# Optimization experiments

Hardware: AMD Instinct MI355X
Metric: run time of the kernel (lower is better)

Reference implementation:

```python
import jax, jax.numpy as jnp
import numpy as np

N = 100000   # nodes
E = 2500000  # edges (before self-loops)
G = 64       # graphs in the batch


def _glorot(key, fi, fo):
    return jax.random.normal(key, (fi, fo), jnp.float32) * jnp.sqrt(2.0 / (fi + fo))


def setup_inputs() -> dict:
    key = jax.random.key(0)
    ks = jax.random.split(key, 8)
    x = jax.random.normal(ks[0], (N, 3), jnp.float32)
    edge_index = jax.random.randint(ks[1], (2, E), 0, N)
    batch = jnp.sort(jax.random.randint(ks[2], (N,), 0, G))
    return dict(
        x=x, edge_index=edge_index, batch=batch,
        W1=_glorot(ks[3], 3, 16),  b1=jnp.zeros((16,), jnp.float32),
        W2=_glorot(ks[4], 16, 32), b2=jnp.zeros((32,), jnp.float32),
        W3=_glorot(ks[5], 32, 16), b3=jnp.zeros((16,), jnp.float32),
        W4=_glorot(ks[6], 16, 2),  b4=jnp.zeros((2,), jnp.float32),
    )


def reference(x, edge_index, batch, W1, b1, W2, b2, W3, b3, W4, b4):
    # PyG GCNConv: add self-loops, sym-normalize by deg^{-1/2}, gather->scatter-add.
    loops = jnp.arange(N)
    src = jnp.concatenate([edge_index[0], loops])  # [E+N]
    dst = jnp.concatenate([edge_index[1], loops])
    deg = jax.ops.segment_sum(jnp.ones_like(dst, jnp.float32), dst, num_segments=N)
    dinv = jax.lax.rsqrt(jnp.maximum(deg, 1.0))  # deg >= 1 due to self-loops
    norm = (dinv[src] * dinv[dst])[:, None]      # [E+N, 1]

    def gcn_conv(h, W, b):
        h = h @ W                                  # [N, out]
        msg = h[src] * norm                        # gather + edge scaling
        agg = jax.ops.segment_sum(msg, dst, num_segments=N)  # scatter-add
        return agg + b

    h = jax.nn.relu(gcn_conv(x, W1, b1))
    h = jax.nn.relu(gcn_conv(h, W2, b2))
    h = jax.nn.relu(gcn_conv(h, W3, b3))
    # F.dropout with training=False (module in eval) is identity
    h = gcn_conv(h, W4, b4)                        # [N, 2]

    # global_mean_pool over graph ids
    sums = jax.ops.segment_sum(h, batch, num_segments=G)
    cnts = jax.ops.segment_sum(jnp.ones((N,), h.dtype), batch, num_segments=G)
    pooled = sums / jnp.maximum(cnts, 1.0)[:, None]  # [G, 2]
    return jax.nn.log_softmax(pooled, axis=1)
```

## Files before the change

kernel.cpp:

```cpp
#include <hip/hip_runtime.h>
#include <hip/hip_fp16.h>
#include <cmath>

static constexpr int NN = 100000;
static constexpr int NE = 2500000;
static constexpr int NG = 64;
static constexpr int NBUCK = (NN + 255) / 256;
static constexpr int CHUNK = 4096;
static constexpr int NCHUNK = (NE + CHUNK - 1) / CHUNK;
static constexpr int CAP = 8192;

union H4 { float2 f2; __half2 h2[2]; };

__device__ inline void unpack_add_fp8x16(float* a, const int4 r) {
    auto f = __builtin_amdgcn_cvt_pk_f32_fp8(r.x, false); a[0] += f[0];  a[1] += f[1];
    f = __builtin_amdgcn_cvt_pk_f32_fp8(r.x, true);       a[2] += f[0];  a[3] += f[1];
    f = __builtin_amdgcn_cvt_pk_f32_fp8(r.y, false);      a[4] += f[0];  a[5] += f[1];
    f = __builtin_amdgcn_cvt_pk_f32_fp8(r.y, true);       a[6] += f[0];  a[7] += f[1];
    f = __builtin_amdgcn_cvt_pk_f32_fp8(r.z, false);      a[8] += f[0];  a[9] += f[1];
    f = __builtin_amdgcn_cvt_pk_f32_fp8(r.z, true);       a[10] += f[0]; a[11] += f[1];
    f = __builtin_amdgcn_cvt_pk_f32_fp8(r.w, false);      a[12] += f[0]; a[13] += f[1];
    f = __builtin_amdgcn_cvt_pk_f32_fp8(r.w, true);       a[14] += f[0]; a[15] += f[1];
}

__device__ inline void store_fp8_pair(unsigned* row_words, int p, float f0, float f1) {
    unsigned my = ((unsigned)__builtin_amdgcn_cvt_pk_fp8_f32(f0, f1, 0, false)) & 0xFFFFu;
    unsigned nb = (unsigned)__shfl_xor((int)my, 1);
    if ((p & 1) == 0) row_words[p >> 1] = my | (nb << 16);
}

__global__ void p1_hist(const int* __restrict__ dst, int* __restrict__ Ht) {
    __shared__ int hist[NBUCK];
    int t = threadIdx.x, c = blockIdx.x;
    for (int i = t; i < NBUCK; i += 256) hist[i] = 0;
    __syncthreads();
    int e0 = c * CHUNK, e1 = min(e0 + CHUNK, NE);
    for (int e = e0 + t; e < e1; e += 256) atomicAdd(&hist[dst[e] >> 8], 1);
    __syncthreads();
    for (int b = t; b < NBUCK; b += 256) Ht[(size_t)b * NCHUNK + c] = hist[b];
}

__global__ void p2_scan(int* __restrict__ Ht, int* __restrict__ count,
                        float* __restrict__ pooled3) {
    __shared__ int s[256];
    int b = blockIdx.x, t = threadIdx.x;
    if (b == 0 && t < NG * 3) pooled3[t] = 0.0f;
    int* row = Ht + (size_t)b * NCHUNK;
    int carry = 0;
    for (int seg = 0; seg < 3; ++seg) {
        int idx = seg * 256 + t;
        int v = (idx < NCHUNK) ? row[idx] : 0;
        __syncthreads();
        s[t] = v;
        __syncthreads();
#pragma unroll
        for (int off = 1; off < 256; off <<= 1) {
            int y = (t >= off) ? s[t - off] : 0;
            __syncthreads();
            s[t] += y;
            __syncthreads();
        }
        int incl = s[t];
        int segtot = s[255];
        if (idx < NCHUNK) row[idx] = incl - v + carry;
        carry += segtot;
    }
    if (t == 0) count[b] = carry;
}

__global__ void p3_scatter(const int* __restrict__ src, const int* __restrict__ dst,
                           const int* __restrict__ Ht, int* __restrict__ staging) {
    __shared__ int cur[NBUCK];
    int t = threadIdx.x, bid = blockIdx.x;
    int x = bid & 7, o = bid >> 3;
    int len = 76 + (x < 3 ? 1 : 0);
    if (o >= len) return;
    int c = x * 76 + min(x, 3) + o;
    for (int b = t; b < NBUCK; b += 256) cur[b] = Ht[(size_t)b * NCHUNK + c];
    __syncthreads();
    int e0 = c * CHUNK, e1 = min(e0 + CHUNK, NE);
    for (int e = e0 + t; e < e1; e += 256) {
        int d = dst[e];
        int b = d >> 8;
        int r = atomicAdd(&cur[b], 1);
        staging[((size_t)b << 13) + r] = src[e] | ((d & 255) << 17);
    }
}

__global__ void csr_build_kernel(const int* __restrict__ staging, const int* __restrict__ count,
                                 const float* __restrict__ x,
                                 unsigned* __restrict__ rsd, float* __restrict__ dinv,
                                 int* __restrict__ csr_src, float2* __restrict__ xsh) {
    __shared__ int hist[256];
    __shared__ int scn[256];
    __shared__ int cur[256];
    int b = blockIdx.x, t = threadIdx.x;
    int cnt = count[b];
    int base = b << 13;
    hist[t] = 0;
    __syncthreads();
    const int* st = staging + ((size_t)b << 13);
    for (int i = t; i < cnt; i += 256) atomicAdd(&hist[st[i] >> 17], 1);
    __syncthreads();
    int h = hist[t];
    scn[t] = h; __syncthreads();
#pragma unroll
    for (int off = 1; off < 256; off <<= 1) {
        int y = (t >= off) ? scn[t - off] : 0;
        __syncthreads();
        scn[t] += y;
        __syncthreads();
    }
    int ex = scn[t] - h;
    int v = (b << 8) + t;
    if (v < NN) {
        float dv = rsqrtf((float)h + 1.0f);
        rsd[v]  = (unsigned)(base + ex) | ((unsigned)h << 23);
        dinv[v] = dv;
        H4 u;
        u.h2[0] = __floats2half2_rn(x[v * 3] * dv, x[v * 3 + 1] * dv);
        u.h2[1] = __floats2half2_rn(x[v * 3 + 2] * dv, 0.0f);
        xsh[v] = u.f2;
    }
    cur[t] = ex;
    __syncthreads();
    for (int i = t; i < cnt; i += 256) {
        int p = st[i];
        int r = atomicAdd(&cur[p >> 17], 1);
        csr_src[base + r] = p & 0x1FFFF;
    }
}

__global__ void __launch_bounds__(256) agg3t1_kernel(const float2* __restrict__ xsh,
        const int* __restrict__ csr, const unsigned* __restrict__ rsd,
        const float* __restrict__ dinv, const float* __restrict__ W1,
        const float* __restrict__ b1, unsigned* __restrict__ g2b) {
    __shared__ float sW1[48], sb1[16];
    int t = threadIdx.x;
    if (t < 48) sW1[t] = W1[t];
    if (t < 16) sb1[t] = b1[t];
    __syncthreads();
    int tid = blockIdx.x * 256 + t;
    int v = tid >> 3, p = tid & 7;
    if (v >= NN) return;
    float a0 = 0.0f, a1 = 0.0f, a2 = 0.0f;
    if (p == 0) {
        H4 u; u.f2 = xsh[v];
        float2 f0 = __half22float2(u.h2[0]), f1 = __half22float2(u.h2[1]);
        a0 = f0.x; a1 = f0.y; a2 = f1.x;
    }
    unsigned rd = rsd[v];
    int s0 = rd & 0x7FFFFF, cnt = (int)(rd >> 23);
    int j = p;
    for (; j + 8 < cnt; j += 16) {
        int s1 = csr[s0 + j];
        int s2 = csr[s0 + j + 8];
        H4 u1; u1.f2 = xsh[s1];
        H4 u2; u2.f2 = xsh[s2];
        float2 f0 = __half22float2(u1.h2[0]), f1 = __half22float2(u1.h2[1]);
        a0 += f0.x; a1 += f0.y; a2 += f1.x;
        f0 = __half22float2(u2.h2[0]); f1 = __half22float2(u2.h2[1]);
        a0 += f0.x; a1 += f0.y; a2 += f1.x;
    }
    if (j < cnt) {
        H4 u; u.f2 = xsh[csr[s0 + j]];
        float2 f0 = __half22float2(u.h2[0]), f1 = __half22float2(u.h2[1]);
        a0 += f0.x; a1 += f0.y; a2 += f1.x;
    }
    a0 += __shfl_xor(a0, 1); a1 += __shfl_xor(a1, 1); a2 += __shfl_xor(a2, 1);
    a0 += __shfl_xor(a0, 2); a1 += __shfl_xor(a1, 2); a2 += __shfl_xor(a2, 2);
    a0 += __shfl_xor(a0, 4); a1 += __shfl_xor(a1, 4); a2 += __shfl_xor(a2, 4);
    float dv = dinv[v];
    a0 *= dv; a1 *= dv; a2 *= dv;
    float f[2];
#pragma unroll
    for (int k = 0; k < 2; ++k) {
        int fo = p * 2 + k;
        float g = fmaf(a0, sW1[fo], fmaf(a1, sW1[16 + fo], fmaf(a2, sW1[32 + fo], sb1[fo])));
        f[k] = fmaxf(g, 0.0f) * dv;
    }
    store_fp8_pair(g2b + (size_t)v * 4, p, f[0], f[1]);
}

__global__ void __launch_bounds__(256) agg16mid_kernel(const int4* __restrict__ g2b,
        const int* __restrict__ csr, const unsigned* __restrict__ rsd,
        const float* __restrict__ dinv, const float* __restrict__ W2,
        const float* __restrict__ b2, const float* __restrict__ W3,
        unsigned* __restrict__ g3b) {
    __shared__ float sW2[512], sW3[512], sb2[32];
    int t = threadIdx.x;
    for (int i = t; i < 512; i += 256) { sW2[i] = W2[i]; sW3[i] = W3[i]; }
    if (t < 32) sb2[t] = b2[t];
    __syncthreads();
    int tid = blockIdx.x * 256 + t;
    int v = tid >> 3, p = tid & 7;
    if (v >= NN) return;
    float a[16];
#pragma unroll
    for (int f = 0; f < 16; ++f) a[f] = 0.0f;
    if (p == 0) unpack_add_fp8x16(a, g2b[v]);
    unsigned rd = rsd[v];
    int s0 = rd & 0x7FFFFF, cnt = (int)(rd >> 23);
    int j = p;
    for (; j + 8 < cnt; j += 16) {
        int s1 = csr[s0 + j];
        int s2 = csr[s0 + j + 8];
        int4 xa = g2b[s1];
        int4 ya = g2b[s2];
        unpack_add_fp8x16(a, xa);
        unpack_add_fp8x16(a, ya);
    }
    if (j < cnt) {
        int4 xa = g2b[csr[s0 + j]];
        unpack_add_fp8x16(a, xa);
    }
#pragma unroll
    for (int f = 0; f < 16; ++f) a[f] += __shfl_xor(a[f], 1);
#pragma unroll
    for (int f = 0; f < 16; ++f) a[f] += __shfl_xor(a[f], 2);
#pragma unroll
    for (int f = 0; f < 16; ++f) a[f] += __shfl_xor(a[f], 4);
    float dv = dinv[v];
#pragma unroll
    for (int f = 0; f < 16; ++f) a[f] *= dv;
    float h2[32];
#pragma unroll
    for (int fo = 0; fo < 32; ++fo) {
        float s = sb2[fo];
#pragma unroll
        for (int fi = 0; fi < 16; ++fi) s = fmaf(a[fi], sW2[fi * 32 + fo], s);
        h2[fo] = fmaxf(s, 0.0f);
    }
    float o[2];
#pragma unroll
    for (int k = 0; k < 2; ++k) {
        int fo = p * 2 + k;
        float s = 0.0f;
#pragma unroll
        for (int fi = 0; fi < 32; ++fi) s = fmaf(h2[fi], sW3[fi * 16 + fo], s);
        o[k] = s * dv;
    }
    store_fp8_pair(g3b + (size_t)v * 4, p, o[0], o[1]);
}

__global__ void __launch_bounds__(256) agg16t4_kernel(const int4* __restrict__ g3b,
        const int* __restrict__ csr, const unsigned* __restrict__ rsd,
        const float* __restrict__ dinv, const float* __restrict__ b3,
        const float* __restrict__ W4, float2* __restrict__ g4) {
    __shared__ float sb3[16], sW4[32];
    int t = threadIdx.x;
    if (t < 16) sb3[t] = b3[t];
    if (t < 32) sW4[t] = W4[t];
    __syncthreads();
    int tid = blockIdx.x * 256 + t;
    int v = tid >> 3, p = tid & 7;
    if (v >= NN) return;
    float a[16];
#pragma unroll
    for (int f = 0; f < 16; ++f) a[f] = 0.0f;
    if (p == 0) unpack_add_fp8x16(a, g3b[v]);
    unsigned rd = rsd[v];
    int s0 = rd & 0x7FFFFF, cnt = (int)(rd >> 23);
    int j = p;
    for (; j + 8 < cnt; j += 16) {
        int s1 = csr[s0 + j];
        int s2 = csr[s0 + j + 8];
        int4 xa = g3b[s1];
        int4 ya = g3b[s2];
        unpack_add_fp8x16(a, xa);
        unpack_add_fp8x16(a, ya);
    }
    if (j < cnt) {
        int4 xa = g3b[csr[s0 + j]];
        unpack_add_fp8x16(a, xa);
    }
#pragma unroll
    for (int f = 0; f < 16; ++f) a[f] += __shfl_xor(a[f], 1);
#pragma unroll
    for (int f = 0; f < 16; ++f) a[f] += __shfl_xor(a[f], 2);
#pragma unroll
    for (int f = 0; f < 16; ++f) a[f] += __shfl_xor(a[f], 4);
    float dv = dinv[v];
    int f0 = p * 2, f1 = p * 2 + 1;
    float h3a = fmaxf(fmaf(a[f0], dv, sb3[f0]), 0.0f);
    float h3b = fmaxf(fmaf(a[f1], dv, sb3[f1]), 0.0f);
    float o0 = fmaf(h3a, sW4[f0 * 2 + 0], h3b * sW4[f1 * 2 + 0]);
    float o1 = fmaf(h3a, sW4[f0 * 2 + 1], h3b * sW4[f1 * 2 + 1]);
    o0 += __shfl_xor(o0, 1); o1 += __shfl_xor(o1, 1);
    o0 += __shfl_xor(o0, 2); o1 += __shfl_xor(o1, 2);
    o0 += __shfl_xor(o0, 4); o1 += __shfl_xor(o1, 4);
    if (p == 0) g4[v] = make_float2(o0 * dv, o1 * dv);
}

__global__ void __launch_bounds__(256) agg2pool_kernel(const float2* __restrict__ g4,
        const int* __restrict__ csr, const unsigned* __restrict__ rsd,
        const float* __restrict__ dinv, const float* __restrict__ b4,
        const int* __restrict__ batch, float* __restrict__ pooled3) {
    __shared__ float spool[NG * 3];
    int t = threadIdx.x;
    for (int i = t; i < NG * 3; i += 256) spool[i] = 0.0f;
    __syncthreads();
    int tid = blockIdx.x * 256 + t;
    int v = tid >> 3, p = tid & 7;
    if (v < NN) {
        float a0 = 0.0f, a1 = 0.0f;
        if (p == 0) { float2 s = g4[v]; a0 = s.x; a1 = s.y; }
        unsigned rd = rsd[v];
        int s0 = rd & 0x7FFFFF, cnt = (int)(rd >> 23);
        int j = p;
        for (; j + 8 < cnt; j += 16) {
            float2 q1 = g4[csr[s0 + j]];
            float2 q2 = g4[csr[s0 + j + 8]];
            a0 += q1.x + q2.x; a1 += q1.y + q2.y;
        }
        if (j < cnt) {
            float2 q = g4[csr[s0 + j]];
            a0 += q.x; a1 += q.y;
        }
        a0 += __shfl_xor(a0, 1); a1 += __shfl_xor(a1, 1);
        a0 += __shfl_xor(a0, 2); a1 += __shfl_xor(a1, 2);
        a0 += __shfl_xor(a0, 4); a1 += __shfl_xor(a1, 4);
        if (p == 0) {
            float dv = dinv[v];
            float o0 = fmaf(a0, dv, b4[0]);
            float o1 = fmaf(a1, dv, b4[1]);
            int gi = batch[v];
            atomicAdd(&spool[gi * 3 + 0], o0);
            atomicAdd(&spool[gi * 3 + 1], o1);
            atomicAdd(&spool[gi * 3 + 2], 1.0f);
        }
    }
    __syncthreads();
    for (int i = t; i < NG * 3; i += 256)
        if (spool[i] != 0.0f) atomicAdd(&pooled3[i], spool[i]);
}

__global__ void lsm_kernel(const float* __restrict__ pooled3, float* __restrict__ out) {
    int g = threadIdx.x;
    if (g < NG) {
        float c = fmaxf(pooled3[g * 3 + 2], 1.0f);
        float a = pooled3[g * 3 + 0] / c;
        float b = pooled3[g * 3 + 1] / c;
        float m = fmaxf(a, b);
        float lse = m + logf(expf(a - m) + expf(b - m));
        out[g * 2 + 0] = a - lse;
        out[g * 2 + 1] = b - lse;
    }
}

extern "C" void kernel_launch(void* const* d_in, const int* in_sizes, int n_in,
                              void* d_out, int out_size, void* d_ws, size_t ws_size,
                              hipStream_t stream) {
    (void)in_sizes; (void)n_in; (void)out_size; (void)ws_size;

    const float* x   = (const float*)d_in[0];
    const int*   ei  = (const int*)d_in[1];
    const int*   bat = (const int*)d_in[2];
    const float* W1  = (const float*)d_in[3];
    const float* b1  = (const float*)d_in[4];
    const float* W2  = (const float*)d_in[5];
    const float* b2  = (const float*)d_in[6];
    const float* W3  = (const float*)d_in[7];
    const float* b3  = (const float*)d_in[8];
    const float* W4  = (const float*)d_in[9];
    const float* b4  = (const float*)d_in[10];
    float* out = (float*)d_out;

    const int* src = ei;
    const int* dst = ei + NE;

    char* w = (char*)d_ws;
    int*      Ht      = (int*)w;      w += ((size_t)NBUCK * NCHUNK * 4 + 15) & ~15ull;
    int*      count   = (int*)w;      w += ((size_t)NBUCK * 4 + 15) & ~15ull;
    int*      staging = (int*)w;      w += (size_t)NBUCK * CAP * 4;
    int*      csr_src = (int*)w;      w += (size_t)NBUCK * CAP * 4;
    unsigned* rsd     = (unsigned*)w; w += (size_t)NN * 4;
    float*    dinv    = (float*)w;    w += (size_t)NN * 4;
    float2*   xsh     = (float2*)w;   w += (size_t)NN * 8;
    unsigned* g2b     = (unsigned*)w; w += (size_t)NN * 16;
    unsigned* g3b     = (unsigned*)w; w += (size_t)NN * 16;
    float2*   g4      = (float2*)w;   w += (size_t)NN * 8;
    float*    pooled3 = (float*)w;    w += NG * 3 * 4;

    const int gN8 = (NN * 8 + 255) / 256;

    p1_hist<<<NCHUNK, 256, 0, stream>>>(dst, Ht);
    p2_scan<<<NBUCK, 256, 0, stream>>>(Ht, count, pooled3);
    p3_scatter<<<616, 256, 0, stream>>>(src, dst, Ht, staging);
    csr_build_kernel<<<NBUCK, 256, 0, stream>>>(staging, count, x, rsd, dinv, csr_src, xsh);

    agg3t1_kernel<<<gN8, 256, 0, stream>>>(xsh, csr_src, rsd, dinv, W1, b1, g2b);
    agg16mid_kernel<<<gN8, 256, 0, stream>>>((const int4*)g2b, csr_src, rsd, dinv, W2, b2,
                                             W3, g3b);
    agg16t4_kernel<<<gN8, 256, 0, stream>>>((const int4*)g3b, csr_src, rsd, dinv, b3, W4, g4);
    agg2pool_kernel<<<gN8, 256, 0, stream>>>(g4, csr_src, rsd, dinv, b4, bat, pooled3);

    lsm_kernel<<<1, 64, 0, stream>>>(pooled3, out);
}
```

Before: 148.6 us.

## Split layer-2/3 dense transform across lanes and fuse log-softmax via ticket

In the middle aggregation kernel, each of the 8 lanes per node now computes only 4 of the 32 hidden features instead of all 32. It then forms partial products against a transposed W3 in shared memory and reduces the 16 outputs with xor shuffles. This removes the redundant 16x32 matvec each lane used to repeat. Separately, the final log-softmax kernel is folded into the pooling kernel with a last-block ticket counter, removing one launch at the cost of a fence and an atomic per block.

```diff
diff --git a/kernel.cpp b/kernel.cpp
--- a/kernel.cpp
+++ b/kernel.cpp
@@ -41,10 +41,11 @@
 }
 
 __global__ void p2_scan(int* __restrict__ Ht, int* __restrict__ count,
-                        float* __restrict__ pooled3) {
+                        float* __restrict__ pooled3, int* __restrict__ ticket) {
     __shared__ int s[256];
     int b = blockIdx.x, t = threadIdx.x;
     if (b == 0 && t < NG * 3) pooled3[t] = 0.0f;
+    if (b == 0 && t == 0) *ticket = 0;
     int* row = Ht + (size_t)b * NCHUNK;
     int carry = 0;
     for (int seg = 0; seg < 3; ++seg) {
@@ -187,9 +188,13 @@
         const float* __restrict__ dinv, const float* __restrict__ W2,
         const float* __restrict__ b2, const float* __restrict__ W3,
         unsigned* __restrict__ g3b) {
-    __shared__ float sW2[512], sW3[512], sb2[32];
+    __shared__ float sW2[512], sW3t[512], sb2[32];
     int t = threadIdx.x;
-    for (int i = t; i < 512; i += 256) { sW2[i] = W2[i]; sW3[i] = W3[i]; }
+    for (int i = t; i < 512; i += 256) {
+        sW2[i] = W2[i];
+        int fo = i >> 5, fi = i & 31;
+        sW3t[i] = W3[fi * 16 + fo];
+    }
     if (t < 32) sb2[t] = b2[t];
     __syncthreads();
     int tid = blockIdx.x * 256 + t;
@@ -223,24 +228,32 @@
     float dv = dinv[v];
 #pragma unroll
     for (int f = 0; f < 16; ++f) a[f] *= dv;
-    float h2[32];
-#pragma unroll
-    for (int fo = 0; fo < 32; ++fo) {
+    float h2p[4];
+#pragma unroll
+    for (int k = 0; k < 4; ++k) {
+        int fo = p * 4 + k;
         float s = sb2[fo];
 #pragma unroll
         for (int fi = 0; fi < 16; ++fi) s = fmaf(a[fi], sW2[fi * 32 + fo], s);
-        h2[fo] = fmaxf(s, 0.0f);
-    }
-    float o[2];
-#pragma unroll
-    for (int k = 0; k < 2; ++k) {
-        int fo = p * 2 + k;
-        float s = 0.0f;
-#pragma unroll
-        for (int fi = 0; fi < 32; ++fi) s = fmaf(h2[fi], sW3[fi * 16 + fo], s);
-        o[k] = s * dv;
-    }
-    store_fp8_pair(g3b + (size_t)v * 4, p, o[0], o[1]);
+        h2p[k] = fmaxf(s, 0.0f);
+    }
+    float po[16];
+#pragma unroll
+    for (int fo = 0; fo < 16; ++fo) {
+        const float* wrow = sW3t + fo * 32 + p * 4;
+        float s = h2p[0] * wrow[0];
+        s = fmaf(h2p[1], wrow[1], s);
+        s = fmaf(h2p[2], wrow[2], s);
+        s = fmaf(h2p[3], wrow[3], s);
+        po[fo] = s;
+    }
+#pragma unroll
+    for (int f = 0; f < 16; ++f) po[f] += __shfl_xor(po[f], 1);
+#pragma unroll
+    for (int f = 0; f < 16; ++f) po[f] += __shfl_xor(po[f], 2);
+#pragma unroll
+    for (int f = 0; f < 16; ++f) po[f] += __shfl_xor(po[f], 4);
+    store_fp8_pair(g3b + (size_t)v * 4, p, po[p * 2] * dv, po[p * 2 + 1] * dv);
 }
 
 __global__ void __launch_bounds__(256) agg16t4_kernel(const int4* __restrict__ g3b,
@@ -295,8 +308,10 @@
 __global__ void __launch_bounds__(256) agg2pool_kernel(const float2* __restrict__ g4,
         const int* __restrict__ csr, const unsigned* __restrict__ rsd,
         const float* __restrict__ dinv, const float* __restrict__ b4,
-        const int* __restrict__ batch, float* __restrict__ pooled3) {
+        const int* __restrict__ batch, float* __restrict__ pooled3,
+        int* __restrict__ ticket, float* __restrict__ out) {
     __shared__ float spool[NG * 3];
+    __shared__ int sdone;
     int t = threadIdx.x;
     for (int i = t; i < NG * 3; i += 256) spool[i] = 0.0f;
     __syncthreads();
@@ -333,18 +348,17 @@
     __syncthreads();
     for (int i = t; i < NG * 3; i += 256)
         if (spool[i] != 0.0f) atomicAdd(&pooled3[i], spool[i]);
-}
-
-__global__ void lsm_kernel(const float* __restrict__ pooled3, float* __restrict__ out) {
-    int g = threadIdx.x;
-    if (g < NG) {
-        float c = fmaxf(pooled3[g * 3 + 2], 1.0f);
-        float a = pooled3[g * 3 + 0] / c;
-        float b = pooled3[g * 3 + 1] / c;
+    __threadfence();
+    if (t == 0) sdone = atomicAdd(ticket, 1);
+    __syncthreads();
+    if (sdone == gridDim.x - 1 && t < NG) {
+        float c = fmaxf(pooled3[t * 3 + 2], 1.0f);
+        float a = pooled3[t * 3 + 0] / c;
+        float b = pooled3[t * 3 + 1] / c;
         float m = fmaxf(a, b);
         float lse = m + logf(expf(a - m) + expf(b - m));
-        out[g * 2 + 0] = a - lse;
-        out[g * 2 + 1] = b - lse;
+        out[t * 2 + 0] = a - lse;
+        out[t * 2 + 1] = b - lse;
     }
 }
 
@@ -381,11 +395,12 @@
     unsigned* g3b     = (unsigned*)w; w += (size_t)NN * 16;
     float2*   g4      = (float2*)w;   w += (size_t)NN * 8;
     float*    pooled3 = (float*)w;    w += NG * 3 * 4;
+    int*      ticket  = (int*)w;      w += 16;
 
     const int gN8 = (NN * 8 + 255) / 256;
 
     p1_hist<<<NCHUNK, 256, 0, stream>>>(dst, Ht);
-    p2_scan<<<NBUCK, 256, 0, stream>>>(Ht, count, pooled3);
+    p2_scan<<<NBUCK, 256, 0, stream>>>(Ht, count, pooled3, ticket);
     p3_scatter<<<616, 256, 0, stream>>>(src, dst, Ht, staging);
     csr_build_kernel<<<NBUCK, 256, 0, stream>>>(staging, count, x, rsd, dinv, csr_src, xsh);
 
@@ -393,7 +408,6 @@
     agg16mid_kernel<<<gN8, 256, 0, stream>>>((const int4*)g2b, csr_src, rsd, dinv, W2, b2,
                                              W3, g3b);
     agg16t4_kernel<<<gN8, 256, 0, stream>>>((const int4*)g3b, csr_src, rsd, dinv, b3, W4, g4);
-    agg2pool_kernel<<<gN8, 256, 0, stream>>>(g4, csr_src, rsd, dinv, b4, bat, pooled3);
-
-    lsm_kernel<<<1, 64, 0, stream>>>(pooled3, out);
-}
+    agg2pool_kernel<<<gN8, 256, 0, stream>>>(g4, csr_src, rsd, dinv, b4, bat, pooled3,
+                                             ticket, out);
+}
```

Result: slower. 323.6 us (+117.7%).
